# Performance work log

Measured on AMD Instinct MI355X. Metric: run time of the kernel, lower is better.

The kernel has to match this reference:

```python
import jax, jax.numpy as jnp
import numpy as np

C_IN, C_OUT = 256, 128

def setup_inputs() -> dict:
    key = jax.random.key(0)
    k1, k2, k3, k4, k5, k6 = jax.random.split(key, 6)
    B, H, W = 8, 64, 64
    p = jax.random.normal(k1, (B, C_IN, H, W), dtype=jnp.float32)
    b = jax.random.normal(k2, (B, C_IN, H, W), dtype=jnp.float32)
    # 1x1 conv weights (Conv2d with kernel 1 == pointwise matmul) + biases
    sq = 1.0 / np.sqrt(C_IN)
    Wq = jax.random.uniform(k3, (C_OUT, C_IN), jnp.float32, -sq, sq)
    bq = jax.random.uniform(k4, (C_OUT,), jnp.float32, -sq, sq)
    Wk = jax.random.uniform(k5, (C_OUT, C_IN), jnp.float32, -sq, sq)
    bk = jax.random.uniform(k6, (C_OUT,), jnp.float32, -sq, sq)
    return {"p": p, "b": b, "Wq": Wq, "bq": bq, "Wk": Wk, "bk": bk}

def reference(p, b, Wq, bq, Wk, bk):
    B, C, H, W = p.shape
    N = H * W
    # 1x1 convs -> flatten spatial dim to N
    q = jnp.einsum('bchw,oc->bhwo', p, Wq) + bq          # [B,H,W,Co]
    q = q.reshape(B, N, -1).astype(jnp.float32)           # [B,N,Co] (query permuted)
    k = jnp.einsum('bchw,oc->bohw', b, Wk) + bk[None, :, None, None]
    k = k.reshape(B, -1, N).astype(jnp.float32)           # [B,Co,N]
    energy = jnp.einsum('bnc,bcm->bnm', q, k)             # [B,N,N] unscaled
    attention = jax.nn.softmax(energy, axis=-1)           # softmax over keys
    value = b.reshape(B, C, N)                            # [B,C,N]
    out = jnp.einsum('bnm,bcm->bcn', attention, value)    # [B,C,N]
    return out.reshape(B, C, H, W)
```

## Files before the change

kernel.cpp:

```cpp
#include <hip/hip_runtime.h>
#include <hip/hip_bf16.h>
#include <math.h>


#define B_   8
#define CIN  256
#define COUT 128
#define NN   4096

typedef _Float16 half8  __attribute__((ext_vector_type(8)));
typedef short    short8 __attribute__((ext_vector_type(8)));
typedef float    f32x4  __attribute__((ext_vector_type(4)));

#define LOG2E 1.44269504088896340736f

__device__ __forceinline__ unsigned short f2bf(float f) {
    union { float f; unsigned u; } v; v.f = f;
    return (unsigned short)((v.u + 0x7FFFu + ((v.u >> 16) & 1u)) >> 16);
}
__device__ __forceinline__ unsigned short f2h(float f) {
    union { _Float16 h; unsigned short u; } v; v.h = (_Float16)f;
    return v.u;
}
__device__ __forceinline__ unsigned int packbf2(float lo, float hi) {
    return (unsigned int)f2bf(lo) | ((unsigned int)f2bf(hi) << 16);
}
__device__ __forceinline__ void dma16(void* lds, const void* g) {
    __builtin_amdgcn_global_load_lds(
        (const __attribute__((address_space(1))) unsigned int*)g,
        (__attribute__((address_space(3))) unsigned int*)lds,
        16, 0, 0);
}

__global__ __launch_bounds__(256) void cvt_w(const float* __restrict__ Wq,
                                             const float* __restrict__ Wk,
                                             const float* __restrict__ bq,
                                             _Float16* __restrict__ Whq,
                                             _Float16* __restrict__ Whk,
                                             float* __restrict__ bqs) {
    const int bx = blockIdx.x, t = threadIdx.x;
    const int isK = (bx >= 32);
    const float* src = isK ? Wk : Wq;
    _Float16* dst = isK ? Whk : Whq;
    const float scale = isK ? 1.0f : LOG2E;
    const int idx = (bx & 31) * 256 + t;
    float4 v = ((const float4*)src)[idx];
    unsigned long long pk = (unsigned long long)f2h(v.x * scale)
                          | ((unsigned long long)f2h(v.y * scale) << 16)
                          | ((unsigned long long)f2h(v.z * scale) << 32)
                          | ((unsigned long long)f2h(v.w * scale) << 48);
    ((unsigned long long*)dst)[idx] = pk;
    if (bx == 0 && t < COUT) bqs[t] = bq[t] * LOG2E;
}

__global__ __launch_bounds__(256) void proj3(const float* __restrict__ X,
                                             const _Float16* __restrict__ Wh,
                                             const float* __restrict__ bias,
                                             _Float16* __restrict__ outN,
                                             _Float16* __restrict__ outT,
                                             unsigned short* __restrict__ Vb)
{
    __shared__ __align__(16) unsigned short T[64 * 264];
    const int bx = blockIdx.x, b = bx >> 6, n0 = (bx & 63) << 6;
    const int t  = threadIdx.x;
    const int cr = t >> 2;
    const int nch = (t & 3) << 4;

#pragma unroll
    for (int it = 0; it < 4; ++it) {
        const int c = it * 64 + cr;
        const float* src = X + ((size_t)(b * CIN + c) * NN + n0 + nch);
        float v[16];
#pragma unroll
        for (int k = 0; k < 4; ++k) {
            float4 f = *(const float4*)(src + k * 4);
            v[k*4] = f.x; v[k*4+1] = f.y; v[k*4+2] = f.z; v[k*4+3] = f.w;
        }
#pragma unroll
        for (int j = 0; j < 16; ++j) T[(nch + j) * 264 + c] = f2h(v[j]);
        if (Vb) {
            unsigned short o[16];
#pragma unroll
            for (int j = 0; j < 16; ++j) o[j] = f2bf(v[j]);
            unsigned short* dst = Vb + (size_t)(b * CIN + c) * NN + n0 + nch;
            *(int4*)dst = *(int4*)o;
            *(int4*)(dst + 8) = *(int4*)(o + 8);
        }
    }
    __syncthreads();

    const int w = t >> 6, lane = t & 63, l15 = lane & 15, quad = lane >> 4, q8 = quad * 8;
    half8 a[8];
#pragma unroll
    for (int s = 0; s < 8; ++s)
        a[s] = *(const half8*)&T[(w * 16 + l15) * 264 + s * 32 + q8];
    f32x4 D[8];
#pragma unroll
    for (int og = 0; og < 8; ++og) D[og] = (f32x4){0.f, 0.f, 0.f, 0.f};
#pragma unroll
    for (int s = 0; s < 8; ++s) {
        const _Float16* wp = Wh + (size_t)l15 * CIN + s * 32 + q8;
#pragma unroll
        for (int og = 0; og < 8; ++og) {
            half8 wf = *(const half8*)(wp + og * 16 * CIN);
            D[og] = __builtin_amdgcn_mfma_f32_16x16x32_f16(a[s], wf, D[og], 0, 0, 0);
        }
    }
    const int nrow = n0 + w * 16 + quad * 4;
    if (outT) {
#pragma unroll
        for (int og = 0; og < 8; ++og) {
            const int o = og * 16 + l15;
            const float bo = bias[o];
            const int c = o >> 3, j = o & 7;
            const int sw = (c & 7) << 2;
#pragma unroll
            for (int r2 = 0; r2 < 4; ++r2) {
                const int n = nrow + r2;
                const int tile = n >> 5, m = n & 31;
                const size_t pos = ((size_t)(b * 128 + tile) * 512
                                    + c * 32 + ((m + sw) & 31)) * 8 + j;
                outT[pos] = (_Float16)(D[og][r2] + bo);
            }
        }
    } else {
#pragma unroll
        for (int og = 0; og < 8; ++og) {
            const int o = og * 16 + l15;
            const float bo = bias[o];
            _Float16* op = outN + ((size_t)(b * NN + nrow) * COUT + o);
#pragma unroll
            for (int r2 = 0; r2 < 4; ++r2)
                op[(size_t)r2 * COUT] = (_Float16)(D[og][r2] + bo);
        }
    }
}

__global__ __launch_bounds__(256, 2) void flash_kernel(const _Float16* __restrict__ Q,
                                                       const _Float16* __restrict__ Ktt,
                                                       const unsigned short* __restrict__ V,
                                                       float* __restrict__ out) {
    __shared__ __align__(16) _Float16       K0sh[32 * 128];
    __shared__ __align__(16) _Float16       K1sh[32 * 128];
    __shared__ __align__(16) unsigned short V0sh[256 * 32];
    __shared__ __align__(16) unsigned short V1sh[256 * 32];
    __shared__ __align__(16) unsigned short Psh[4 * 16 * 40];

    const int bx   = blockIdx.x;
    const int b    = bx >> 6;
    const int q0   = (bx & 63) << 6;
    const int t    = threadIdx.x;
    const int w    = t >> 6;
    const int lane = t & 63;
    const int l15  = lane & 15;
    const int quad = lane >> 4;
    const int q8   = quad * 8;

    const _Float16* Qg = Q + (size_t)b * NN * COUT;
    const _Float16* Kb = Ktt + (size_t)b * 128 * 4096;
    const unsigned short* Vg = V + (size_t)b * CIN * NN;

    half8 Qf[4];
    {
        const _Float16* qr = Qg + (size_t)(q0 + w * 16 + l15) * COUT;
#pragma unroll
        for (int s = 0; s < 4; ++s)
            Qf[s] = *(const half8*)(qr + s * 32 + q8);
    }

    f32x4 O[16];
#pragma unroll
    for (int i = 0; i < 16; ++i) O[i] = (f32x4){0.f, 0.f, 0.f, 0.f};
    float lsum[4] = {0.f, 0.f, 0.f, 0.f};

    unsigned short* pw = Psh + w * 640;
    const int vrow0 = w * 64 + (lane >> 2);
    const int vch8  = (lane & 3) * 8;

    auto issue = [&](int kt, _Float16* Kd, unsigned short* Vd) {
        const _Float16* gk = Kb + (size_t)kt * 4096;
        dma16(Kd + (w * 2 + 0) * 512, gk + (w * 2 + 0) * 512 + lane * 8);
        dma16(Kd + (w * 2 + 1) * 512, gk + (w * 2 + 1) * 512 + lane * 8);
        const int k0 = kt << 5;
#pragma unroll
        for (int i = 0; i < 4; ++i)
            dma16(Vd + (w * 64 + i * 16) * 32,
                  Vg + (size_t)(vrow0 + i * 16) * NN + k0 + vch8);
    };

    auto step = [&](int kt, const _Float16* Kc, const unsigned short* Vc,
                    _Float16* Kn, unsigned short* Vn) {
        if (kt + 1 < 128) issue(kt + 1, Kn, Vn);

        f32x4 S0 = {0.f, 0.f, 0.f, 0.f}, S1 = {0.f, 0.f, 0.f, 0.f};
#pragma unroll
        for (int s = 0; s < 4; ++s) {
            const int c  = 4 * s + quad;
            const int sw = (c & 7) << 2;
            const int x0 = (l15 + sw) & 31;
            half8 kf0 = *(const half8*)(Kc + (c * 32 + x0) * 8);
            half8 kf1 = *(const half8*)(Kc + (c * 32 + (x0 ^ 16)) * 8);
            S0 = __builtin_amdgcn_mfma_f32_16x16x32_f16(Qf[s], kf0, S0, 0, 0, 0);
            S1 = __builtin_amdgcn_mfma_f32_16x16x32_f16(Qf[s], kf1, S1, 0, 0, 0);
        }

        f32x4 E0, E1;
#pragma unroll
        for (int r = 0; r < 4; ++r) {
            E0[r] = exp2f(S0[r]);
            E1[r] = exp2f(S1[r]);
            lsum[r] += E0[r] + E1[r];
        }
        {
            f32x4 P0, P1;
#pragma unroll
            for (int r = 0; r < 4; ++r) { P0[r] = __shfl_xor(E0[r], 1); P1[r] = __shfl_xor(E1[r], 1); }
            const int odd = l15 & 1;
            unsigned short* wp0 = pw + (((quad << 2) + (odd << 1)) * 40) + (l15 & ~1);
            unsigned int pk0 = packbf2(odd ? P0[2] : E0[0], odd ? E0[2] : P0[0]);
            unsigned int pk1 = packbf2(odd ? P0[3] : E0[1], odd ? E0[3] : P0[1]);
            unsigned int pk2 = packbf2(odd ? P1[2] : E1[0], odd ? E1[2] : P1[0]);
            unsigned int pk3 = packbf2(odd ? P1[3] : E1[1], odd ? E1[3] : P1[1]);
            *(unsigned int*)&wp0[0]  = pk0;
            *(unsigned int*)&wp0[40] = pk1;
            *(unsigned int*)&wp0[16] = pk2;
            *(unsigned int*)&wp0[56] = pk3;
        }

        {
            short8 pf = *(const short8*)(pw + l15 * 40 + q8);
            const unsigned short* vb0 = Vc + l15 * 32 + q8;
#pragma unroll
            for (int cg = 0; cg < 16; ++cg) {
                short8 vf = *(const short8*)(vb0 + cg * 512);
                O[cg] = __builtin_amdgcn_mfma_f32_16x16x32_bf16(pf, vf, O[cg], 0, 0, 0);
            }
        }
        __syncthreads();
    };

    issue(0, K0sh, V0sh);
    __syncthreads();
#pragma unroll 1
    for (int kt = 0; kt < 128; kt += 2) {
        step(kt,     K0sh, V0sh, K1sh, V1sh);
        step(kt + 1, K1sh, V1sh, K0sh, V0sh);
    }

    float inv[4];
#pragma unroll
    for (int r = 0; r < 4; ++r) {
        float s = lsum[r];
        s += __shfl_xor(s, 1);
        s += __shfl_xor(s, 2);
        s += __shfl_xor(s, 4);
        s += __shfl_xor(s, 8);
        inv[r] = 1.0f / s;
    }
    float* ob = out + (size_t)b * CIN * NN + q0 + w * 16 + quad * 4;
#pragma unroll
    for (int cg = 0; cg < 16; ++cg) {
        const int c = cg * 16 + l15;
#pragma unroll
        for (int r = 0; r < 4; ++r)
            ob[(size_t)c * NN + r] = O[cg][r] * inv[r];
    }
}

extern "C" void kernel_launch(void* const* d_in, const int* in_sizes, int n_in,
                              void* d_out, int out_size, void* d_ws, size_t ws_size,
                              hipStream_t stream) {
    const float* p  = (const float*)d_in[0];
    const float* bv = (const float*)d_in[1];
    const float* Wq = (const float*)d_in[2];
    const float* bq = (const float*)d_in[3];
    const float* Wk = (const float*)d_in[4];
    const float* bk = (const float*)d_in[5];
    float* outp = (float*)d_out;

    char* ws = (char*)d_ws;
    const size_t szQ = (size_t)B_ * NN * COUT * 2;
    const size_t szV = (size_t)B_ * NN * CIN * 2;
    const size_t szW = (size_t)COUT * CIN * 2;
    _Float16*       Qh  = (_Float16*)ws;
    _Float16*       Ktt = (_Float16*)(ws + szQ);
    unsigned short* Vb  = (unsigned short*)(ws + 2 * szQ);
    _Float16*       Whq = (_Float16*)(ws + 2 * szQ + szV);
    _Float16*       Whk = (_Float16*)(ws + 2 * szQ + szV + szW);
    float*          bqs = (float*)(ws + 2 * szQ + szV + 2 * szW);

    cvt_w<<<64, 256, 0, stream>>>(Wq, Wk, bq, Whq, Whk, bqs);
    proj3<<<512, 256, 0, stream>>>(p,  Whq, bqs, Qh, (_Float16*)nullptr, (unsigned short*)nullptr);
    proj3<<<512, 256, 0, stream>>>(bv, Whk, bk,  (_Float16*)nullptr, Ktt, Vb);
    flash_kernel<<<512, 256, 0, stream>>>(Qh, Ktt, Vb, outp);
}
```

Measured before the change: 312.2 us.

## Split PV matmul by channel per wave and share P tile across waves

Each wave now computes the output for all 64 queries of the block but only its own 64-channel slice, instead of 16 queries across all 256 channels. Every wave therefore reads the full P tile from shared memory, while each V fragment is loaded once and reused across four MFMAs. This adds a block-wide barrier between writing P and the PV product, and the V prefetch is moved to after that barrier. The V shared-memory layout is re-swizzled to avoid bank conflicts, and row sums now go through shared memory so the final store can write 16-byte vectors contiguous along N.

```diff
diff --git a/kernel.cpp b/kernel.cpp
--- a/kernel.cpp
+++ b/kernel.cpp
@@ -144,7 +144,8 @@
     __shared__ __align__(16) _Float16       K1sh[32 * 128];
     __shared__ __align__(16) unsigned short V0sh[256 * 32];
     __shared__ __align__(16) unsigned short V1sh[256 * 32];
-    __shared__ __align__(16) unsigned short Psh[4 * 16 * 40];
+    __shared__ __align__(16) unsigned short Psh[64 * 40];
+    __shared__ __align__(16) float          Lsh[64];
 
     const int bx   = blockIdx.x;
     const int b    = bx >> 6;
@@ -173,33 +174,37 @@
     for (int i = 0; i < 16; ++i) O[i] = (f32x4){0.f, 0.f, 0.f, 0.f};
     float lsum[4] = {0.f, 0.f, 0.f, 0.f};
 
-    unsigned short* pw = Psh + w * 640;
-    const int vrow0 = w * 64 + (lane >> 2);
-    const int vch8  = (lane & 3) * 8;
-
-    auto issue = [&](int kt, _Float16* Kd, unsigned short* Vd) {
+    const int vmq   = ((lane & 3) - ((lane >> 3) & 3)) & 3;
+    const int vcrow = lane >> 2;
+    const int vslot = (quad + (l15 >> 1)) & 3;
+
+    auto issueK = [&](int kt, _Float16* Kd) {
         const _Float16* gk = Kb + (size_t)kt * 4096;
         dma16(Kd + (w * 2 + 0) * 512, gk + (w * 2 + 0) * 512 + lane * 8);
         dma16(Kd + (w * 2 + 1) * 512, gk + (w * 2 + 1) * 512 + lane * 8);
+    };
+    auto issueV = [&](int kt, unsigned short* Vd) {
         const int k0 = kt << 5;
 #pragma unroll
-        for (int i = 0; i < 4; ++i)
-            dma16(Vd + (w * 64 + i * 16) * 32,
-                  Vg + (size_t)(vrow0 + i * 16) * NN + k0 + vch8);
+        for (int i = 0; i < 4; ++i) {
+            const int cc = (w * 4 + i) * 16 + vcrow;
+            dma16(Vd + (w * 4 + i) * 512,
+                  Vg + (size_t)cc * NN + k0 + vmq * 8);
+        }
     };
 
-    auto step = [&](int kt, const _Float16* Kc, const unsigned short* Vc,
-                    _Float16* Kn, unsigned short* Vn) {
-        if (kt + 1 < 128) issue(kt + 1, Kn, Vn);
+    auto halfstep = [&](int kt, const _Float16* Kc, const unsigned short* Vc,
+                        _Float16* Kn, unsigned short* Vn) {
+        if (kt + 1 < 128) issueK(kt + 1, Kn);
 
         f32x4 S0 = {0.f, 0.f, 0.f, 0.f}, S1 = {0.f, 0.f, 0.f, 0.f};
 #pragma unroll
         for (int s = 0; s < 4; ++s) {
-            const int c  = 4 * s + quad;
-            const int sw = (c & 7) << 2;
+            const int kc = 4 * s + quad;
+            const int sw = (kc & 7) << 2;
             const int x0 = (l15 + sw) & 31;
-            half8 kf0 = *(const half8*)(Kc + (c * 32 + x0) * 8);
-            half8 kf1 = *(const half8*)(Kc + (c * 32 + (x0 ^ 16)) * 8);
+            half8 kf0 = *(const half8*)(Kc + (kc * 32 + x0) * 8);
+            half8 kf1 = *(const half8*)(Kc + (kc * 32 + (x0 ^ 16)) * 8);
             S0 = __builtin_amdgcn_mfma_f32_16x16x32_f16(Qf[s], kf0, S0, 0, 0, 0);
             S1 = __builtin_amdgcn_mfma_f32_16x16x32_f16(Qf[s], kf1, S1, 0, 0, 0);
         }
@@ -216,7 +221,8 @@
 #pragma unroll
             for (int r = 0; r < 4; ++r) { P0[r] = __shfl_xor(E0[r], 1); P1[r] = __shfl_xor(E1[r], 1); }
             const int odd = l15 & 1;
-            unsigned short* wp0 = pw + (((quad << 2) + (odd << 1)) * 40) + (l15 & ~1);
+            unsigned short* wp0 = Psh + w * 640
+                                + (((quad << 2) + (odd << 1)) * 40) + (l15 & ~1);
             unsigned int pk0 = packbf2(odd ? P0[2] : E0[0], odd ? E0[2] : P0[0]);
             unsigned int pk1 = packbf2(odd ? P0[3] : E0[1], odd ? E0[3] : P0[1]);
             unsigned int pk2 = packbf2(odd ? P1[2] : E1[0], odd ? E1[2] : P1[0]);
@@ -227,27 +233,37 @@
             *(unsigned int*)&wp0[56] = pk3;
         }
 
+        __syncthreads();
+
+        if (kt + 1 < 128) issueV(kt + 1, Vn);
+
         {
-            short8 pf = *(const short8*)(pw + l15 * 40 + q8);
-            const unsigned short* vb0 = Vc + l15 * 32 + q8;
-#pragma unroll
-            for (int cg = 0; cg < 16; ++cg) {
-                short8 vf = *(const short8*)(vb0 + cg * 512);
-                O[cg] = __builtin_amdgcn_mfma_f32_16x16x32_bf16(pf, vf, O[cg], 0, 0, 0);
+            short8 pf[4];
+#pragma unroll
+            for (int ni = 0; ni < 4; ++ni)
+                pf[ni] = *(const short8*)(Psh + (ni * 16 + l15) * 40 + q8);
+            const unsigned short* vb = Vc + (w * 64 + l15) * 32 + vslot * 8;
+#pragma unroll
+            for (int cj = 0; cj < 4; ++cj) {
+                short8 vf = *(const short8*)(vb + cj * 512);
+#pragma unroll
+                for (int ni = 0; ni < 4; ++ni)
+                    O[ni * 4 + cj] = __builtin_amdgcn_mfma_f32_16x16x32_bf16(pf[ni], vf, O[ni * 4 + cj], 0, 0, 0);
             }
         }
+
         __syncthreads();
     };
 
-    issue(0, K0sh, V0sh);
+    issueK(0, K0sh);
+    issueV(0, V0sh);
     __syncthreads();
 #pragma unroll 1
     for (int kt = 0; kt < 128; kt += 2) {
-        step(kt,     K0sh, V0sh, K1sh, V1sh);
-        step(kt + 1, K1sh, V1sh, K0sh, V0sh);
-    }
-
-    float inv[4];
+        halfstep(kt,     K0sh, V0sh, K1sh, V1sh);
+        halfstep(kt + 1, K1sh, V1sh, K0sh, V0sh);
+    }
+
 #pragma unroll
     for (int r = 0; r < 4; ++r) {
         float s = lsum[r];
@@ -255,15 +271,25 @@
         s += __shfl_xor(s, 2);
         s += __shfl_xor(s, 4);
         s += __shfl_xor(s, 8);
-        inv[r] = 1.0f / s;
-    }
-    float* ob = out + (size_t)b * CIN * NN + q0 + w * 16 + quad * 4;
-#pragma unroll
-    for (int cg = 0; cg < 16; ++cg) {
-        const int c = cg * 16 + l15;
-#pragma unroll
-        for (int r = 0; r < 4; ++r)
-            ob[(size_t)c * NN + r] = O[cg][r] * inv[r];
+        if (l15 == 0) Lsh[w * 16 + (quad << 2) + r] = s;
+    }
+    __syncthreads();
+    float* ob = out + (size_t)b * CIN * NN + q0;
+#pragma unroll
+    for (int ni = 0; ni < 4; ++ni) {
+        const f32x4 lv = *(const f32x4*)&Lsh[ni * 16 + (quad << 2)];
+        f32x4 linv;
+#pragma unroll
+        for (int r = 0; r < 4; ++r) linv[r] = 1.0f / lv[r];
+        const int nb = ni * 16 + (quad << 2);
+#pragma unroll
+        for (int cj = 0; cj < 4; ++cj) {
+            const int c = w * 64 + cj * 16 + l15;
+            f32x4 val = O[ni * 4 + cj];
+#pragma unroll
+            for (int r = 0; r < 4; ++r) val[r] *= linv[r];
+            *(f32x4*)(ob + (size_t)c * NN + nb) = val;
+        }
     }
 }
 
```

After: 305.5 us. 2.2% less time.
